# Kernel optimization log

Hardware: AMD Instinct MI355X
Metric: run time of the kernel (lower is better)

The kernel has to match this reference:

```python
import jax, jax.numpy as jnp
import numpy as np

B = 16
L = 3600
LATENT = 64
D_MODEL = 128
D_INNER = 256   # expand * d_model
D_STATE = 16
D_CONV = 4
DT_RANK = 8     # ceil(d_model / 16)


def setup_inputs() -> dict:
    key = jax.random.key(0)
    ks = jax.random.split(key, 10)

    def w(k, shape, fan_in):
        return jax.random.normal(k, shape, jnp.float32) / np.float32(np.sqrt(fan_in))

    return {
        "z_sequence": jax.random.normal(ks[0], (B, L, LATENT), jnp.float32),
        # embedding Linear(latent_dim -> mamba_dim)
        "emb_w": w(ks[1], (D_MODEL, LATENT), LATENT),
        "emb_b": jnp.zeros((D_MODEL,), jnp.float32),
        # Mamba in_proj (no bias): d_model -> 2*d_inner
        "in_proj_w": w(ks[2], (2 * D_INNER, D_MODEL), D_MODEL),
        # depthwise causal conv1d (d_inner groups, kernel d_conv) + bias
        "conv_w": w(ks[3], (D_INNER, 1, D_CONV), D_CONV),
        "conv_b": jnp.zeros((D_INNER,), jnp.float32),
        # x_proj (no bias): d_inner -> dt_rank + 2*d_state
        "x_proj_w": w(ks[4], (DT_RANK + 2 * D_STATE, D_INNER), D_INNER),
        # dt_proj: dt_rank -> d_inner, bias init so softplus(b) ~ 0.01
        "dt_proj_w": w(ks[5], (D_INNER, DT_RANK), DT_RANK),
        "dt_proj_b": jnp.full((D_INNER,), np.log(np.expm1(0.01)), jnp.float32),
        # S4D-real init: A = -[1..d_state] per channel
        "A_log": jnp.log(jnp.broadcast_to(
            jnp.arange(1, D_STATE + 1, dtype=jnp.float32), (D_INNER, D_STATE))),
        "D_skip": jnp.ones((D_INNER,), jnp.float32),
        # out_proj (no bias): d_inner -> d_model
        "out_proj_w": w(ks[6], (D_MODEL, D_INNER), D_INNER),
        # LayerNorm(d_model)
        "norm_w": jnp.ones((D_MODEL,), jnp.float32),
        "norm_b": jnp.zeros((D_MODEL,), jnp.float32),
        # classifier Linear(d_model -> 1)
        "cls_w": w(ks[7], (1, D_MODEL), D_MODEL),
        "cls_b": jnp.zeros((1,), jnp.float32),
    }


def _forward(z_sequence, emb_w, emb_b, in_proj_w, conv_w, conv_b, x_proj_w,
             dt_proj_w, dt_proj_b, A_log, D_skip, out_proj_w,
             norm_w, norm_b, cls_w, cls_b):
    silu = jax.nn.silu
    # embedding: (B,L,latent) -> (B,L,d_model)
    x_emb = z_sequence @ emb_w.T + emb_b
    # Mamba in_proj -> x, z  each (B,L,d_inner)
    xz = x_emb @ in_proj_w.T
    x, z = jnp.split(xz, 2, axis=-1)
    # causal depthwise conv over time
    x_ncl = x.transpose(0, 2, 1)  # (B, d_inner, L)
    x_conv = jax.lax.conv_general_dilated(
        x_ncl, conv_w, window_strides=(1,), padding=[(D_CONV - 1, 0)],
        feature_group_count=D_INNER, dimension_numbers=("NCH", "OIH", "NCH"))
    x = silu(x_conv.transpose(0, 2, 1) + conv_b)  # (B,L,d_inner)
    # input-dependent SSM params
    x_dbl = x @ x_proj_w.T  # (B,L,dt_rank+2*d_state)
    dt_in, B_ssm, C_ssm = jnp.split(x_dbl, [DT_RANK, DT_RANK + D_STATE], axis=-1)
    dt = jax.nn.softplus(dt_in @ dt_proj_w.T + dt_proj_b)  # (B,L,d_inner)
    A = -jnp.exp(A_log)  # (d_inner, d_state)

    def step(h, inp):
        x_t, dt_t, B_t, C_t = inp  # (B,d_inner),(B,d_inner),(B,d_state),(B,d_state)
        h = jnp.exp(dt_t[:, :, None] * A) * h + (dt_t * x_t)[:, :, None] * B_t[:, None, :]
        y = jnp.einsum("bds,bs->bd", h, C_t)
        return h, y

    h0 = jnp.zeros((x.shape[0], D_INNER, D_STATE), x.dtype)
    xs = (x.transpose(1, 0, 2), dt.transpose(1, 0, 2),
          B_ssm.transpose(1, 0, 2), C_ssm.transpose(1, 0, 2))
    _, ys = jax.lax.scan(step, h0, xs)  # ys: (L,B,d_inner)
    y = ys.transpose(1, 0, 2) + x * D_skip
    y = y * silu(z)
    out = y @ out_proj_w.T  # (B,L,d_model)
    # take last timestep, LayerNorm, classify
    x_last = out[:, -1, :]
    mu = x_last.mean(-1, keepdims=True)
    var = ((x_last - mu) ** 2).mean(-1, keepdims=True)
    xn = (x_last - mu) / jnp.sqrt(var + 1e-5) * norm_w + norm_b
    logit = xn @ cls_w.T + cls_b  # (B,1)
    return logit.squeeze(-1)      # (B,)


def reference(z_sequence, emb_w, emb_b, in_proj_w, conv_w, conv_b, x_proj_w,
              dt_proj_w, dt_proj_b, A_log, D_skip, out_proj_w,
              norm_w, norm_b, cls_w, cls_b):
    return _forward(z_sequence, emb_w, emb_b, in_proj_w, conv_w, conv_b,
                    x_proj_w, dt_proj_w, dt_proj_b, A_log, D_skip,
                    out_proj_w, norm_w, norm_b, cls_w, cls_b)
```

## Files before the change

kernel.cpp:

```cpp
#include <hip/hip_runtime.h>
#include <hip/hip_bf16.h>
#include <math.h>

#define B_  16
#define L_  3600
#define LAT 64
#define DM  128
#define DI  256
#define DS  16
#define DR  8

#define TT  45
#define NT  80
#define TC  100
#define NC  36
#define THR (-20.0f)

typedef __bf16 v8bf __attribute__((ext_vector_type(8)));
typedef float  v4f  __attribute__((ext_vector_type(4)));
typedef unsigned short v8us __attribute__((ext_vector_type(8)));

#define MFMA16(A, Bf, C) __builtin_amdgcn_mfma_f32_16x16x32_bf16((A), (Bf), (C), 0, 0, 0)

__device__ __forceinline__ float siluf(float v) {
    return v * __builtin_amdgcn_rcpf(1.0f + __expf(-v));
}
__device__ __forceinline__ float softplusf(float v) {
    float r = __logf(1.0f + __expf(v));
    return (v > 15.0f) ? v : r;
}
__device__ __forceinline__ float bf2f(unsigned short u) {
    unsigned int x = ((unsigned int)u) << 16;
    return __builtin_bit_cast(float, x);
}
__device__ __forceinline__ unsigned short f2bf(float f) {
    __hip_bfloat16 h = __float2bfloat16(f);
    return __builtin_bit_cast(unsigned short, h);
}

__global__ __launch_bounds__(64) void k0_combine(
    const float* __restrict__ in_proj_w, const float* __restrict__ emb_w,
    const float* __restrict__ emb_b, float* __restrict__ W1, float* __restrict__ b1)
{
    int d = blockIdx.x, k = threadIdx.x;
    const float* row = in_proj_w + (size_t)d * DM;
    float acc = 0.f;
    for (int m = 0; m < DM; ++m) acc += row[m] * emb_w[m * LAT + k];
    W1[d * LAT + k] = acc;
    if (k == 0) {
        float ab = 0.f;
        for (int m = 0; m < DM; ++m) ab += row[m] * emb_b[m];
        b1[d] = ab;
    }
}

__global__ __launch_bounds__(256, 2) void k1_front(
    const float* __restrict__ z, const float* __restrict__ conv_w,
    const float* __restrict__ conv_b, const float* __restrict__ x_proj_w,
    const float* __restrict__ W1, const float* __restrict__ b1,
    float* __restrict__ dtin, float* __restrict__ Bssm,
    __hip_bfloat16* __restrict__ x_bf)
{
    __shared__ float xpre[48 * 258];
    __shared__ unsigned short uB[12288];

    int b = blockIdx.y, tile = blockIdx.x;
    int t0 = tile * TT;
    int t0m3 = t0 - 3;
    int tid = threadIdx.x;
    int lane = tid & 63, wid = tid >> 6;
    int l15 = lane & 15, l4 = lane >> 4;

    float4 cw = *(const float4*)(conv_w + tid * 4);
    float cb = conv_b[tid];
    float bias = b1[tid];

    v8bf wh[4][2], wl[4][2];
    {
        int d0w = wid * 64;
        #pragma unroll
        for (int nt = 0; nt < 4; ++nt) {
            int dr = d0w + nt * 16 + l15;
            const float* wrow = W1 + (size_t)dr * LAT;
            #pragma unroll
            for (int kb = 0; kb < 2; ++kb) {
                int k0 = kb * 32 + l4 * 8;
                float4 u = *(const float4*)(wrow + k0);
                float4 v = *(const float4*)(wrow + k0 + 4);
                float f[8] = {u.x, u.y, u.z, u.w, v.x, v.y, v.z, v.w};
                v8us hh, ll;
                #pragma unroll
                for (int i = 0; i < 8; ++i) {
                    unsigned short h = f2bf(f[i]);
                    hh[i] = h;
                    ll[i] = f2bf(f[i] - bf2f(h));
                }
                wh[nt][kb] = __builtin_bit_cast(v8bf, hh);
                wl[nt][kb] = __builtin_bit_cast(v8bf, ll);
            }
        }
    }

    {
        const float* zb = z + (size_t)b * L_ * LAT;
        for (int i = tid; i < 48 * 8; i += 256) {
            int r = i >> 3, s = i & 7;
            int tg = t0m3 + r;
            float f[8];
            if (tg >= 0) {
                float4 u = *(const float4*)(zb + (size_t)tg * LAT + s * 8);
                float4 v = *(const float4*)(zb + (size_t)tg * LAT + s * 8 + 4);
                f[0]=u.x; f[1]=u.y; f[2]=u.z; f[3]=u.w; f[4]=v.x; f[5]=v.y; f[6]=v.z; f[7]=v.w;
            } else {
                #pragma unroll
                for (int q = 0; q < 8; ++q) f[q] = 0.f;
            }
            v8us hh, ll;
            #pragma unroll
            for (int q = 0; q < 8; ++q) {
                unsigned short h = f2bf(f[q]);
                hh[q] = h;
                ll[q] = f2bf(f[q] - bf2f(h));
            }
            int idx = r * 64 + ((s * 8) ^ ((r & 7) << 3));
            *(v8us*)&uB[idx] = hh;
            *(v8us*)&uB[3072 + idx] = ll;
        }
    }
    __syncthreads();

    {
        int d0w = wid * 64;
        #pragma unroll
        for (int mt = 0; mt < 3; ++mt) {
            int r = mt * 16 + l15;
            int sw = (r & 7) << 3;
            int kb0 = l4 * 8;
            v8bf ah0 = __builtin_bit_cast(v8bf, *(const v8us*)&uB[r * 64 + (kb0 ^ sw)]);
            v8bf ah1 = __builtin_bit_cast(v8bf, *(const v8us*)&uB[r * 64 + ((32 + kb0) ^ sw)]);
            v8bf al0 = __builtin_bit_cast(v8bf, *(const v8us*)&uB[3072 + r * 64 + (kb0 ^ sw)]);
            v8bf al1 = __builtin_bit_cast(v8bf, *(const v8us*)&uB[3072 + r * 64 + ((32 + kb0) ^ sw)]);
            int rr = mt * 16 + l4 * 4;
            #pragma unroll
            for (int nt = 0; nt < 4; ++nt) {
                v4f acc = {0.f, 0.f, 0.f, 0.f};
                acc = MFMA16(ah0, wh[nt][0], acc);
                acc = MFMA16(ah1, wh[nt][1], acc);
                acc = MFMA16(ah0, wl[nt][0], acc);
                acc = MFMA16(ah1, wl[nt][1], acc);
                acc = MFMA16(al0, wh[nt][0], acc);
                acc = MFMA16(al1, wh[nt][1], acc);
                int cc = d0w + nt * 16 + l15;
                xpre[(rr + 0) * 258 + cc] = acc[0];
                xpre[(rr + 1) * 258 + cc] = acc[1];
                xpre[(rr + 2) * 258 + cc] = acc[2];
                xpre[(rr + 3) * 258 + cc] = acc[3];
            }
        }
    }

    float4 xwreg[6];
    {
        #pragma unroll
        for (int p = 0; p < 3; ++p) {
            int i = tid + p * 256;
            int j = i >> 5, s = i & 31;
            const float* src = x_proj_w + (size_t)j * DI + s * 8;
            xwreg[2 * p]     = *(const float4*)(src);
            xwreg[2 * p + 1] = *(const float4*)(src + 4);
        }
    }
    __syncthreads();

    float xr[TT];
    {
        int d = tid;
        float p0 = xpre[0 * 258 + d] + ((t0m3 + 0 >= 0) ? bias : 0.f);
        float p1 = xpre[1 * 258 + d] + ((t0m3 + 1 >= 0) ? bias : 0.f);
        float p2 = xpre[2 * 258 + d] + ((t0m3 + 2 >= 0) ? bias : 0.f);
        #pragma unroll
        for (int r = 3; r < 48; ++r) {
            float cur = xpre[r * 258 + d] + bias;
            float xc = cw.x * p0 + cw.y * p1 + cw.z * p2 + cw.w * cur + cb;
            xr[r - 3] = siluf(xc);
            p0 = p1; p1 = p2; p2 = cur;
        }
        __hip_bfloat16* xb = x_bf + ((size_t)b * L_ + t0) * DI + d;
        #pragma unroll
        for (int t = 0; t < TT; ++t)
            xb[(size_t)t * DI] = __float2bfloat16(xr[t]);
    }
    __syncthreads();

    unsigned short* xt16 = (unsigned short*)xpre;
    {
        int d = tid;
        #pragma unroll
        for (int t = 0; t < TT; ++t)
            xt16[t * 512 + (d ^ ((t & 7) << 3))] = f2bf(xr[t]);
        #pragma unroll
        for (int t = TT; t < 48; ++t)
            xt16[t * 512 + (d ^ ((t & 7) << 3))] = 0;
        #pragma unroll
        for (int p = 0; p < 3; ++p) {
            int i = tid + p * 256;
            int j = i >> 5, s = i & 31;
            float4 u = xwreg[2 * p], v = xwreg[2 * p + 1];
            float f[8] = {u.x, u.y, u.z, u.w, v.x, v.y, v.z, v.w};
            v8us hh, ll;
            #pragma unroll
            for (int q = 0; q < 8; ++q) {
                unsigned short h = f2bf(f[q]);
                hh[q] = h;
                ll[q] = f2bf(f[q] - bf2f(h));
            }
            int idx = j * 256 + ((s * 8) ^ ((j & 7) << 3));
            *(v8us*)&uB[idx] = hh;
            *(v8us*)&uB[6144 + idx] = ll;
        }
    }
    __syncthreads();

    if (wid < 3) {
        int mt = wid;
        int rA = mt * 16 + l15;
        int swA = (rA & 7) << 3;
        int jc0 = l15;
        int jc1 = 16 + l15; if (jc1 > 23) jc1 = 23;
        v4f acc0 = {0.f, 0.f, 0.f, 0.f}, acc1 = {0.f, 0.f, 0.f, 0.f};
        #pragma unroll
        for (int kb = 0; kb < 8; ++kb) {
            int k0 = kb * 32 + l4 * 8;
            v8bf xa  = __builtin_bit_cast(v8bf, *(const v8us*)&xt16[rA * 512 + (k0 ^ swA)]);
            int s0 = k0 ^ ((jc0 & 7) << 3);
            int s1 = k0 ^ ((jc1 & 7) << 3);
            v8bf b0h = __builtin_bit_cast(v8bf, *(const v8us*)&uB[jc0 * 256 + s0]);
            v8bf b0l = __builtin_bit_cast(v8bf, *(const v8us*)&uB[6144 + jc0 * 256 + s0]);
            v8bf b1h = __builtin_bit_cast(v8bf, *(const v8us*)&uB[jc1 * 256 + s1]);
            v8bf b1l = __builtin_bit_cast(v8bf, *(const v8us*)&uB[6144 + jc1 * 256 + s1]);
            acc0 = MFMA16(xa, b0h, acc0);
            acc0 = MFMA16(xa, b0l, acc0);
            acc1 = MFMA16(xa, b1h, acc1);
            acc1 = MFMA16(xa, b1l, acc1);
        }
        int rr = mt * 16 + l4 * 4;
        #pragma unroll
        for (int reg = 0; reg < 4; ++reg) {
            int t = rr + reg;
            if (t < TT) {
                size_t tg = (size_t)b * L_ + (t0 + t);
                float v0 = acc0[reg], v1 = acc1[reg];
                if (l15 < 8) {
                    dtin[tg * DR + l15] = v0;
                    Bssm[tg * DS + 8 + l15] = v1;
                } else {
                    Bssm[tg * DS + (l15 - 8)] = v0;
                }
            }
        }
    }
}

__global__ __launch_bounds__(256) void k3a_chunksums(
    const float* __restrict__ dtin, const float* __restrict__ dt_proj_w,
    const float* __restrict__ dt_proj_b, float* __restrict__ Dcs,
    __hip_bfloat16* __restrict__ dt_bf)
{
    int c = blockIdx.x, b = blockIdx.y, d = threadIdx.x;
    int t0 = c * TC;
    const float4* wp = (const float4*)(dt_proj_w + (size_t)d * DR);
    float4 wA = wp[0], wB = wp[1];
    float bias = dt_proj_b[d];
    const float* din = dtin + ((size_t)b * L_ + t0) * DR;
    __hip_bfloat16* dout = dt_bf + ((size_t)b * L_ + t0) * DI + d;
    float S = 0.f;
    for (int t = 0; t < TC; ++t) {
        const float4* dr = (const float4*)(din + (size_t)t * DR);
        float4 u = dr[0], v = dr[1];
        float r = bias + u.x*wA.x + u.y*wA.y + u.z*wA.z + u.w*wA.w
                       + v.x*wB.x + v.y*wB.y + v.z*wB.z + v.w*wB.w;
        float dt = softplusf(r);
        dout[(size_t)t * DI] = __float2bfloat16(dt);
        S += dt;
    }
    Dcs[((size_t)b * NC + c) * DI + d] = S;
}

__global__ __launch_bounds__(256) void k3a2_suffix(
    const float* __restrict__ Dcs, float* __restrict__ Rsuf)
{
    int b = blockIdx.x, d = threadIdx.x;
    float R = 0.f;
    for (int c = NC - 1; c >= 0; --c) {
        Rsuf[((size_t)b * NC + c) * DI + d] = R;
        R += Dcs[((size_t)b * NC + c) * DI + d];
    }
}

__global__ __launch_bounds__(512) void k3b_scan(
    const __hip_bfloat16* __restrict__ x_bf, const __hip_bfloat16* __restrict__ dt_bf,
    const float* __restrict__ Bssm, const float* __restrict__ A_log,
    const float* __restrict__ Rsuf, float* __restrict__ hpart)
{
    int c = blockIdx.x, dg = blockIdx.y, b = blockIdx.z;
    int tid = threadIdx.x;
    int dh = tid & 31;
    int s  = ((tid >> 6) << 1) | ((tid >> 5) & 1);
    int d  = dg * 32 + dh;

    float a = -__expf(A_log[d * DS + s]);
    float R = Rsuf[((size_t)b * NC + c) * DI + d];
    size_t hoff = (((size_t)c * B_ + b) * DS + s) * DI + d;

    float H = 0.f;
    float S_run = R;
    if (!__all(a * R < THR)) {
        int t0 = c * TC;
        const __hip_bfloat16* xp = x_bf + ((size_t)b * L_ + t0) * DI + d;
        const __hip_bfloat16* dp = dt_bf + ((size_t)b * L_ + t0) * DI + d;
        const float* Bp = Bssm + ((size_t)b * L_ + t0) * DS + s;
        for (int j = TC - 4; j >= 0; j -= 4) {
            float x3 = __bfloat162float(xp[(j+3)*DI]);
            float x2 = __bfloat162float(xp[(j+2)*DI]);
            float x1 = __bfloat162float(xp[(j+1)*DI]);
            float x0 = __bfloat162float(xp[(j+0)*DI]);
            float d3 = __bfloat162float(dp[(j+3)*DI]);
            float d2 = __bfloat162float(dp[(j+2)*DI]);
            float d1 = __bfloat162float(dp[(j+1)*DI]);
            float d0 = __bfloat162float(dp[(j+0)*DI]);
            float B3 = Bp[(j+3)*DS];
            float B2 = Bp[(j+2)*DS];
            float B1 = Bp[(j+1)*DS];
            float B0 = Bp[(j+0)*DS];
            float e;
            e = __expf(a * S_run); H = fmaf(e * d3 * x3, B3, H); S_run += d3;
            e = __expf(a * S_run); H = fmaf(e * d2 * x2, B2, H); S_run += d2;
            e = __expf(a * S_run); H = fmaf(e * d1 * x1, B1, H); S_run += d1;
            e = __expf(a * S_run); H = fmaf(e * d0 * x0, B0, H); S_run += d0;
            if (__all(a * S_run < THR)) break;
        }
    }
    hpart[hoff] = H;
}

__global__ __launch_bounds__(256) void k3c_comb(
    const float* __restrict__ hpart, float* __restrict__ h_last)
{
    int id = blockIdx.x * 256 + threadIdx.x;
    float acc = 0.f;
    for (int c = 0; c < NC; ++c) acc += hpart[(size_t)c * (B_ * DS * DI) + id];
    int d = id & (DI - 1);
    int s = (id >> 8) & (DS - 1);
    int b = id >> 12;
    h_last[((size_t)b * DI + d) * DS + s] = acc;
}

__global__ __launch_bounds__(256) void k4_final(
    const float* __restrict__ z, const float* __restrict__ emb_w,
    const float* __restrict__ emb_b, const float* __restrict__ in_proj_w,
    const float* __restrict__ conv_w, const float* __restrict__ conv_b,
    const float* __restrict__ x_proj_w, const float* __restrict__ D_skip,
    const float* __restrict__ out_proj_w, const float* __restrict__ norm_w,
    const float* __restrict__ norm_b, const float* __restrict__ cls_w,
    const float* __restrict__ cls_b, const float* __restrict__ W1,
    const float* __restrict__ b1, const float* __restrict__ h_last,
    float* __restrict__ out)
{
    __shared__ float zl[4][64];
    __shared__ float xlast[DI];
    __shared__ float xemb[DM];
    __shared__ float Cl[DS];
    __shared__ float ylds[DI];
    __shared__ float olds[DM];
    int b = blockIdx.x, tid = threadIdx.x;
    {
        int r = tid >> 6, k = tid & 63;
        zl[r][k] = z[((size_t)b * L_ + (L_ - 4 + r)) * LAT + k];
    }
    __syncthreads();
    {
        int d = tid;
        const float* wr = W1 + d * LAT;
        float xp[4];
        #pragma unroll
        for (int r = 0; r < 4; ++r) {
            float acc = b1[d];
            for (int k = 0; k < LAT; ++k) acc += zl[r][k] * wr[k];
            xp[r] = acc;
        }
        float4 cwv = *(const float4*)(conv_w + d * 4);
        float xc = cwv.x*xp[0] + cwv.y*xp[1] + cwv.z*xp[2] + cwv.w*xp[3] + conv_b[d];
        xlast[d] = siluf(xc);
    }
    __syncthreads();
    if (tid < DS) {
        float acc = 0.f;
        const float* wr = x_proj_w + (size_t)(DR + DS + tid) * DI;
        for (int k = 0; k < DI; ++k) acc += xlast[k] * wr[k];
        Cl[tid] = acc;
    }
    if (tid >= 64 && tid < 64 + DM) {
        int m = tid - 64;
        float acc = emb_b[m];
        const float* wr = emb_w + (size_t)m * LAT;
        for (int k = 0; k < LAT; ++k) acc += zl[3][k] * wr[k];
        xemb[m] = acc;
    }
    __syncthreads();
    {
        int d = tid;
        const float* hr = h_last + ((size_t)b * DI + d) * DS;
        float hs = 0.f;
        #pragma unroll
        for (int si = 0; si < DS; ++si) hs += hr[si] * Cl[si];
        float y = hs + xlast[d] * D_skip[d];
        float zbv = 0.f;
        const float* wr = in_proj_w + (size_t)(DI + d) * DM;
        for (int m = 0; m < DM; ++m) zbv += xemb[m] * wr[m];
        y *= siluf(zbv);
        ylds[d] = y;
    }
    __syncthreads();
    if (tid < DM) {
        float acc = 0.f;
        const float* wr = out_proj_w + (size_t)tid * DI;
        for (int k = 0; k < DI; ++k) acc += ylds[k] * wr[k];
        olds[tid] = acc;
    }
    __syncthreads();
    if (tid < 64) {
        float v0 = olds[tid], v1 = olds[tid + 64];
        float sum = v0 + v1;
        #pragma unroll
        for (int off = 32; off > 0; off >>= 1) sum += __shfl_down(sum, off);
        float mu = __shfl(sum, 0) * (1.0f / 128.0f);
        float dv0 = v0 - mu, dv1 = v1 - mu;
        float vs = dv0 * dv0 + dv1 * dv1;
        #pragma unroll
        for (int off = 32; off > 0; off >>= 1) vs += __shfl_down(vs, off);
        float var = __shfl(vs, 0) * (1.0f / 128.0f);
        float rstd = rsqrtf(var + 1e-5f);
        float xn0 = dv0 * rstd * norm_w[tid] + norm_b[tid];
        float xn1 = dv1 * rstd * norm_w[tid + 64] + norm_b[tid + 64];
        float lg = xn0 * cls_w[tid] + xn1 * cls_w[tid + 64];
        #pragma unroll
        for (int off = 32; off > 0; off >>= 1) lg += __shfl_down(lg, off);
        if (tid == 0) out[b] = lg + cls_b[0];
    }
}

extern "C" void kernel_launch(void* const* d_in, const int* in_sizes, int n_in,
                              void* d_out, int out_size, void* d_ws, size_t ws_size,
                              hipStream_t stream) {
    (void)in_sizes; (void)n_in; (void)out_size;
    const float* z         = (const float*)d_in[0];
    const float* emb_w     = (const float*)d_in[1];
    const float* emb_b     = (const float*)d_in[2];
    const float* in_proj_w = (const float*)d_in[3];
    const float* conv_w    = (const float*)d_in[4];
    const float* conv_b    = (const float*)d_in[5];
    const float* x_proj_w  = (const float*)d_in[6];
    const float* dt_proj_w = (const float*)d_in[7];
    const float* dt_proj_b = (const float*)d_in[8];
    const float* A_log     = (const float*)d_in[9];
    const float* D_skip    = (const float*)d_in[10];
    const float* out_proj_w= (const float*)d_in[11];
    const float* norm_w    = (const float*)d_in[12];
    const float* norm_b    = (const float*)d_in[13];
    const float* cls_w     = (const float*)d_in[14];
    const float* cls_b     = (const float*)d_in[15];
    float* out = (float*)d_out;

    float* ws    = (float*)d_ws;
    float* W1    = ws;
    float* b1    = W1 + 16384;
    float* dtin  = b1 + 256;
    float* Bssm  = dtin + 460800;
    float* Dcs   = Bssm + 921600;
    float* Rsuf  = Dcs + 147456;
    float* hpart = Rsuf + 147456;
    float* hlast = hpart + 2359296;
    float* fend  = hlast + 65536;
    __hip_bfloat16* x_bf  = (__hip_bfloat16*)fend;
    __hip_bfloat16* dt_bf = x_bf + (size_t)B_ * L_ * DI;
    size_t needed = ((size_t)(16384 + 256 + 460800 + 921600 + 147456 + 147456 + 2359296 + 65536)) * 4
                  + (size_t)B_ * L_ * DI * 2 * 2;
    if (ws_size < needed) return;

    k0_combine   <<<dim3(DI),        dim3(LAT), 0, stream>>>(in_proj_w, emb_w, emb_b, W1, b1);
    k1_front     <<<dim3(NT, B_),    dim3(256), 0, stream>>>(z, conv_w, conv_b, x_proj_w, W1, b1, dtin, Bssm, x_bf);
    k3a_chunksums<<<dim3(NC, B_),    dim3(256), 0, stream>>>(dtin, dt_proj_w, dt_proj_b, Dcs, dt_bf);
    k3a2_suffix  <<<dim3(B_),        dim3(256), 0, stream>>>(Dcs, Rsuf);
    k3b_scan     <<<dim3(NC, 8, B_), dim3(512), 0, stream>>>(x_bf, dt_bf, Bssm, A_log, Rsuf, hpart);
    k3c_comb     <<<dim3(256),       dim3(256), 0, stream>>>(hpart, hlast);
    k4_final     <<<dim3(B_),        dim3(256), 0, stream>>>(z, emb_w, emb_b, in_proj_w, conv_w, conv_b,
                                                             x_proj_w, D_skip, out_proj_w, norm_w, norm_b,
                                                             cls_w, cls_b, W1, b1, hlast, out);
}
```

Before: 130.3 us.

## Fuse dt projection into front kernel, precompute split-bf16 weights, atomically combine scan chunks

The dt_proj plus softplus and the per-chunk dt sums move into k1_front, so the dtin round trip through global memory and the separate k3a kernel go away. Chunk size becomes 45 to match the front tile. The hi/lo bf16 weight splits for W1 and x_proj are precomputed once in k0, so each k1 block no longer recomputes them. The k3c reduction kernel and the hpart buffer are replaced by atomicAdd into a zeroed hlast with a new [b][s][d] layout. This trades fewer launches and less traffic for 80 chunks of suffix work instead of 36, and for atomic contention; zeroing hlast in k1 depends on k1 finishing before k3b starts.

```diff
diff --git a/kernel.cpp b/kernel.cpp
--- a/kernel.cpp
+++ b/kernel.cpp
@@ -12,8 +12,8 @@
 
 #define TT  45
 #define NT  80
-#define TC  100
-#define NC  36
+#define NC  80
+#define TC  45
 #define THR (-20.0f)
 
 typedef __bf16 v8bf __attribute__((ext_vector_type(8)));
@@ -40,29 +40,55 @@
 
 __global__ __launch_bounds__(64) void k0_combine(
     const float* __restrict__ in_proj_w, const float* __restrict__ emb_w,
-    const float* __restrict__ emb_b, float* __restrict__ W1, float* __restrict__ b1)
+    const float* __restrict__ emb_b, const float* __restrict__ x_proj_w,
+    float* __restrict__ W1, float* __restrict__ b1,
+    unsigned short* __restrict__ W1h, unsigned short* __restrict__ W1l,
+    unsigned short* __restrict__ xwh, unsigned short* __restrict__ xwl)
 {
-    int d = blockIdx.x, k = threadIdx.x;
-    const float* row = in_proj_w + (size_t)d * DM;
-    float acc = 0.f;
-    for (int m = 0; m < DM; ++m) acc += row[m] * emb_w[m * LAT + k];
-    W1[d * LAT + k] = acc;
-    if (k == 0) {
-        float ab = 0.f;
-        for (int m = 0; m < DM; ++m) ab += row[m] * emb_b[m];
-        b1[d] = ab;
+    int blk = blockIdx.x, k = threadIdx.x;
+    if (blk < DI) {
+        int d = blk;
+        const float* row = in_proj_w + (size_t)d * DM;
+        float acc = 0.f;
+        for (int m = 0; m < DM; ++m) acc += row[m] * emb_w[m * LAT + k];
+        W1[d * LAT + k] = acc;
+        unsigned short h = f2bf(acc);
+        W1h[d * LAT + k] = h;
+        W1l[d * LAT + k] = f2bf(acc - bf2f(h));
+        if (k == 0) {
+            float ab = 0.f;
+            for (int m = 0; m < DM; ++m) ab += row[m] * emb_b[m];
+            b1[d] = ab;
+        }
+    } else {
+        int j = blk - DI;
+        int sw = (j & 7) << 3;
+        #pragma unroll
+        for (int q = 0; q < 4; ++q) {
+            int c = k * 4 + q;
+            float v = x_proj_w[(size_t)j * DI + c];
+            unsigned short h = f2bf(v);
+            int idx = j * 256 + (c ^ sw);
+            xwh[idx] = h;
+            xwl[idx] = f2bf(v - bf2f(h));
+        }
     }
 }
 
 __global__ __launch_bounds__(256, 2) void k1_front(
     const float* __restrict__ z, const float* __restrict__ conv_w,
-    const float* __restrict__ conv_b, const float* __restrict__ x_proj_w,
-    const float* __restrict__ W1, const float* __restrict__ b1,
-    float* __restrict__ dtin, float* __restrict__ Bssm,
-    __hip_bfloat16* __restrict__ x_bf)
+    const float* __restrict__ conv_b, const float* __restrict__ dt_proj_w,
+    const float* __restrict__ dt_proj_b,
+    const unsigned short* __restrict__ W1h, const unsigned short* __restrict__ W1l,
+    const unsigned short* __restrict__ xwh, const unsigned short* __restrict__ xwl,
+    const float* __restrict__ b1,
+    float* __restrict__ Bssm, float* __restrict__ Dcs,
+    __hip_bfloat16* __restrict__ x_bf, __hip_bfloat16* __restrict__ dt_bf,
+    float* __restrict__ hlast)
 {
     __shared__ float xpre[48 * 258];
     __shared__ unsigned short uB[12288];
+    __shared__ float dtl[TT][8];
 
     int b = blockIdx.y, tile = blockIdx.x;
     int t0 = tile * TT;
@@ -71,9 +97,19 @@
     int lane = tid & 63, wid = tid >> 6;
     int l15 = lane & 15, l4 = lane >> 4;
 
+    if (tile == 0) {
+        float4 z4 = make_float4(0.f, 0.f, 0.f, 0.f);
+        float4* hl4 = (float4*)(hlast + (size_t)b * (DS * DI));
+        #pragma unroll
+        for (int i = 0; i < 4; ++i) hl4[tid + i * 256] = z4;
+    }
+
     float4 cw = *(const float4*)(conv_w + tid * 4);
     float cb = conv_b[tid];
     float bias = b1[tid];
+    float4 dwA = *(const float4*)(dt_proj_w + (size_t)tid * DR);
+    float4 dwB = *(const float4*)(dt_proj_w + (size_t)tid * DR + 4);
+    float dbias = dt_proj_b[tid];
 
     v8bf wh[4][2], wl[4][2];
     {
@@ -81,22 +117,11 @@
         #pragma unroll
         for (int nt = 0; nt < 4; ++nt) {
             int dr = d0w + nt * 16 + l15;
-            const float* wrow = W1 + (size_t)dr * LAT;
             #pragma unroll
             for (int kb = 0; kb < 2; ++kb) {
                 int k0 = kb * 32 + l4 * 8;
-                float4 u = *(const float4*)(wrow + k0);
-                float4 v = *(const float4*)(wrow + k0 + 4);
-                float f[8] = {u.x, u.y, u.z, u.w, v.x, v.y, v.z, v.w};
-                v8us hh, ll;
-                #pragma unroll
-                for (int i = 0; i < 8; ++i) {
-                    unsigned short h = f2bf(f[i]);
-                    hh[i] = h;
-                    ll[i] = f2bf(f[i] - bf2f(h));
-                }
-                wh[nt][kb] = __builtin_bit_cast(v8bf, hh);
-                wl[nt][kb] = __builtin_bit_cast(v8bf, ll);
+                wh[nt][kb] = __builtin_bit_cast(v8bf, *(const v8us*)(W1h + (size_t)dr * LAT + k0));
+                wl[nt][kb] = __builtin_bit_cast(v8bf, *(const v8us*)(W1l + (size_t)dr * LAT + k0));
             }
         }
     }
@@ -159,15 +184,12 @@
         }
     }
 
-    float4 xwreg[6];
+    v8us xwr[6];
     {
         #pragma unroll
         for (int p = 0; p < 3; ++p) {
-            int i = tid + p * 256;
-            int j = i >> 5, s = i & 31;
-            const float* src = x_proj_w + (size_t)j * DI + s * 8;
-            xwreg[2 * p]     = *(const float4*)(src);
-            xwreg[2 * p + 1] = *(const float4*)(src + 4);
+            xwr[p]     = *(const v8us*)(xwh + tid * 24 + p * 8);
+            xwr[3 + p] = *(const v8us*)(xwl + tid * 24 + p * 8);
         }
     }
     __syncthreads();
@@ -203,20 +225,8 @@
             xt16[t * 512 + (d ^ ((t & 7) << 3))] = 0;
         #pragma unroll
         for (int p = 0; p < 3; ++p) {
-            int i = tid + p * 256;
-            int j = i >> 5, s = i & 31;
-            float4 u = xwreg[2 * p], v = xwreg[2 * p + 1];
-            float f[8] = {u.x, u.y, u.z, u.w, v.x, v.y, v.z, v.w};
-            v8us hh, ll;
-            #pragma unroll
-            for (int q = 0; q < 8; ++q) {
-                unsigned short h = f2bf(f[q]);
-                hh[q] = h;
-                ll[q] = f2bf(f[q] - bf2f(h));
-            }
-            int idx = j * 256 + ((s * 8) ^ ((j & 7) << 3));
-            *(v8us*)&uB[idx] = hh;
-            *(v8us*)&uB[6144 + idx] = ll;
+            *(v8us*)&uB[tid * 24 + p * 8] = xwr[p];
+            *(v8us*)&uB[6144 + tid * 24 + p * 8] = xwr[3 + p];
         }
     }
     __syncthreads();
@@ -251,7 +261,7 @@
                 size_t tg = (size_t)b * L_ + (t0 + t);
                 float v0 = acc0[reg], v1 = acc1[reg];
                 if (l15 < 8) {
-                    dtin[tg * DR + l15] = v0;
+                    dtl[t][l15] = v0;
                     Bssm[tg * DS + 8 + l15] = v1;
                 } else {
                     Bssm[tg * DS + (l15 - 8)] = v0;
@@ -259,31 +269,24 @@
             }
         }
     }
-}
-
-__global__ __launch_bounds__(256) void k3a_chunksums(
-    const float* __restrict__ dtin, const float* __restrict__ dt_proj_w,
-    const float* __restrict__ dt_proj_b, float* __restrict__ Dcs,
-    __hip_bfloat16* __restrict__ dt_bf)
-{
-    int c = blockIdx.x, b = blockIdx.y, d = threadIdx.x;
-    int t0 = c * TC;
-    const float4* wp = (const float4*)(dt_proj_w + (size_t)d * DR);
-    float4 wA = wp[0], wB = wp[1];
-    float bias = dt_proj_b[d];
-    const float* din = dtin + ((size_t)b * L_ + t0) * DR;
-    __hip_bfloat16* dout = dt_bf + ((size_t)b * L_ + t0) * DI + d;
-    float S = 0.f;
-    for (int t = 0; t < TC; ++t) {
-        const float4* dr = (const float4*)(din + (size_t)t * DR);
-        float4 u = dr[0], v = dr[1];
-        float r = bias + u.x*wA.x + u.y*wA.y + u.z*wA.z + u.w*wA.w
-                       + v.x*wB.x + v.y*wB.y + v.z*wB.z + v.w*wB.w;
-        float dt = softplusf(r);
-        dout[(size_t)t * DI] = __float2bfloat16(dt);
-        S += dt;
-    }
-    Dcs[((size_t)b * NC + c) * DI + d] = S;
+    __syncthreads();
+
+    {
+        int d = tid;
+        __hip_bfloat16* dout = dt_bf + ((size_t)b * L_ + t0) * DI + d;
+        float S = 0.f;
+        #pragma unroll 5
+        for (int t = 0; t < TT; ++t) {
+            float4 u = *(const float4*)&dtl[t][0];
+            float4 v = *(const float4*)&dtl[t][4];
+            float r = dbias + u.x*dwA.x + u.y*dwA.y + u.z*dwA.z + u.w*dwA.w
+                            + v.x*dwB.x + v.y*dwB.y + v.z*dwB.z + v.w*dwB.w;
+            float dt = softplusf(r);
+            dout[(size_t)t * DI] = __float2bfloat16(dt);
+            S += dt;
+        }
+        Dcs[((size_t)b * NC + tile) * DI + d] = S;
+    }
 }
 
 __global__ __launch_bounds__(256) void k3a2_suffix(
@@ -300,7 +303,7 @@
 __global__ __launch_bounds__(512) void k3b_scan(
     const __hip_bfloat16* __restrict__ x_bf, const __hip_bfloat16* __restrict__ dt_bf,
     const float* __restrict__ Bssm, const float* __restrict__ A_log,
-    const float* __restrict__ Rsuf, float* __restrict__ hpart)
+    const float* __restrict__ Rsuf, float* __restrict__ hlast)
 {
     int c = blockIdx.x, dg = blockIdx.y, b = blockIdx.z;
     int tid = threadIdx.x;
@@ -310,7 +313,6 @@
 
     float a = -__expf(A_log[d * DS + s]);
     float R = Rsuf[((size_t)b * NC + c) * DI + d];
-    size_t hoff = (((size_t)c * B_ + b) * DS + s) * DI + d;
 
     float H = 0.f;
     float S_run = R;
@@ -319,7 +321,13 @@
         const __hip_bfloat16* xp = x_bf + ((size_t)b * L_ + t0) * DI + d;
         const __hip_bfloat16* dp = dt_bf + ((size_t)b * L_ + t0) * DI + d;
         const float* Bp = Bssm + ((size_t)b * L_ + t0) * DS + s;
-        for (int j = TC - 4; j >= 0; j -= 4) {
+        {
+            float x4 = __bfloat162float(xp[(TC-1)*DI]);
+            float d4 = __bfloat162float(dp[(TC-1)*DI]);
+            float B4 = Bp[(TC-1)*DS];
+            float e = __expf(a * S_run); H = fmaf(e * d4 * x4, B4, H); S_run += d4;
+        }
+        for (int j = TC - 5; j >= 0; j -= 4) {
             float x3 = __bfloat162float(xp[(j+3)*DI]);
             float x2 = __bfloat162float(xp[(j+2)*DI]);
             float x1 = __bfloat162float(xp[(j+1)*DI]);
@@ -340,19 +348,8 @@
             if (__all(a * S_run < THR)) break;
         }
     }
-    hpart[hoff] = H;
-}
-
-__global__ __launch_bounds__(256) void k3c_comb(
-    const float* __restrict__ hpart, float* __restrict__ h_last)
-{
-    int id = blockIdx.x * 256 + threadIdx.x;
-    float acc = 0.f;
-    for (int c = 0; c < NC; ++c) acc += hpart[(size_t)c * (B_ * DS * DI) + id];
-    int d = id & (DI - 1);
-    int s = (id >> 8) & (DS - 1);
-    int b = id >> 12;
-    h_last[((size_t)b * DI + d) * DS + s] = acc;
+    if (H != 0.f)
+        atomicAdd(hlast + (((size_t)b * DS + s) * DI + d), H);
 }
 
 __global__ __launch_bounds__(256) void k4_final(
@@ -409,10 +406,10 @@
     __syncthreads();
     {
         int d = tid;
-        const float* hr = h_last + ((size_t)b * DI + d) * DS;
         float hs = 0.f;
         #pragma unroll
-        for (int si = 0; si < DS; ++si) hs += hr[si] * Cl[si];
+        for (int si = 0; si < DS; ++si)
+            hs += h_last[((size_t)b * DS + si) * DI + d] * Cl[si];
         float y = hs + xlast[d] * D_skip[d];
         float zbv = 0.f;
         const float* wr = in_proj_w + (size_t)(DI + d) * DM;
@@ -474,26 +471,30 @@
     float* ws    = (float*)d_ws;
     float* W1    = ws;
     float* b1    = W1 + 16384;
-    float* dtin  = b1 + 256;
-    float* Bssm  = dtin + 460800;
+    float* Bssm  = b1 + 256;
     float* Dcs   = Bssm + 921600;
-    float* Rsuf  = Dcs + 147456;
-    float* hpart = Rsuf + 147456;
-    float* hlast = hpart + 2359296;
+    float* Rsuf  = Dcs + 327680;
+    float* hlast = Rsuf + 327680;
     float* fend  = hlast + 65536;
-    __hip_bfloat16* x_bf  = (__hip_bfloat16*)fend;
+    unsigned short* W1h  = (unsigned short*)fend;
+    unsigned short* W1l  = W1h + 16384;
+    unsigned short* xwh  = W1l + 16384;
+    unsigned short* xwl  = xwh + 6144;
+    __hip_bfloat16* x_bf  = (__hip_bfloat16*)(xwl + 6144);
     __hip_bfloat16* dt_bf = x_bf + (size_t)B_ * L_ * DI;
-    size_t needed = ((size_t)(16384 + 256 + 460800 + 921600 + 147456 + 147456 + 2359296 + 65536)) * 4
+    size_t needed = ((size_t)(16384 + 256 + 921600 + 327680 + 327680 + 65536)) * 4
+                  + ((size_t)(16384 + 16384 + 6144 + 6144)) * 2
                   + (size_t)B_ * L_ * DI * 2 * 2;
     if (ws_size < needed) return;
 
-    k0_combine   <<<dim3(DI),        dim3(LAT), 0, stream>>>(in_proj_w, emb_w, emb_b, W1, b1);
-    k1_front     <<<dim3(NT, B_),    dim3(256), 0, stream>>>(z, conv_w, conv_b, x_proj_w, W1, b1, dtin, Bssm, x_bf);
-    k3a_chunksums<<<dim3(NC, B_),    dim3(256), 0, stream>>>(dtin, dt_proj_w, dt_proj_b, Dcs, dt_bf);
-    k3a2_suffix  <<<dim3(B_),        dim3(256), 0, stream>>>(Dcs, Rsuf);
-    k3b_scan     <<<dim3(NC, 8, B_), dim3(512), 0, stream>>>(x_bf, dt_bf, Bssm, A_log, Rsuf, hpart);
-    k3c_comb     <<<dim3(256),       dim3(256), 0, stream>>>(hpart, hlast);
-    k4_final     <<<dim3(B_),        dim3(256), 0, stream>>>(z, emb_w, emb_b, in_proj_w, conv_w, conv_b,
+    k0_combine <<<dim3(DI + 24),     dim3(LAT), 0, stream>>>(in_proj_w, emb_w, emb_b, x_proj_w,
+                                                             W1, b1, W1h, W1l, xwh, xwl);
+    k1_front   <<<dim3(NT, B_),      dim3(256), 0, stream>>>(z, conv_w, conv_b, dt_proj_w, dt_proj_b,
+                                                             W1h, W1l, xwh, xwl, b1,
+                                                             Bssm, Dcs, x_bf, dt_bf, hlast);
+    k3a2_suffix<<<dim3(B_),          dim3(256), 0, stream>>>(Dcs, Rsuf);
+    k3b_scan   <<<dim3(NC, 8, B_),   dim3(512), 0, stream>>>(x_bf, dt_bf, Bssm, A_log, Rsuf, hlast);
+    k4_final   <<<dim3(B_),          dim3(256), 0, stream>>>(z, emb_w, emb_b, in_proj_w, conv_w, conv_b,
                                                              x_proj_w, D_skip, out_proj_w, norm_w, norm_b,
                                                              cls_w, cls_b, W1, b1, hlast, out);
 }
```

Measured after the change: 121.6 us. -6.7%, faster.
